# Kernel optimization log

Measured on AMD Instinct MI355X. Metric: run time of the kernel, lower is better.

## Reference

```python
import jax, jax.numpy as jnp
import numpy as np

NEG_SLOPE = 0.2


def setup_inputs() -> dict:
    key = jax.random.key(0)
    k1, k2 = jax.random.split(key)
    N, D = 8192, 64
    Wh = jax.random.normal(k1, (N, D), dtype=jnp.float32)
    # xavier_uniform on (2D, 1): bound = sqrt(6/(2D+1))
    bound = float(np.sqrt(6.0 / (2 * D + 1)))
    a = jax.random.uniform(k2, (2 * D, 1), dtype=jnp.float32, minval=-bound, maxval=bound)
    return {"Wh": Wh, "a": a}


def reference(Wh, a):
    # Original: e = LeakyReLU(cat([Wh_i, Wh_j]) @ a).view(N, N)
    # Equivalent: split a into halves; score(i,j) = Wh[i]@a1 + Wh[j]@a2.
    D = Wh.shape[1]
    a1 = a[:D, 0]  # [D]
    a2 = a[D:, 0]  # [D]
    s1 = Wh @ a1   # [N] row contribution (Wh_i)
    s2 = Wh @ a2   # [N] col contribution (Wh_j)
    e = s1[:, None] + s2[None, :]  # [N, N]
    return jnp.where(e >= 0, e, NEG_SLOPE * e)
```

## Files before the change

kernel.cpp:

```cpp
#include <hip/hip_runtime.h>

#define NEG_SLOPE 0.2f
#define D 64

__global__ __launch_bounds__(256) void gemv2_kernel(const float* __restrict__ Wh,
                                                    const float* __restrict__ a,
                                                    float* __restrict__ s,
                                                    int N) {
    const int gtid = blockIdx.x * blockDim.x + threadIdx.x;
    const int row  = gtid >> 6;
    const int lane = threadIdx.x & 63;
    if (row >= N) return;

    const float w  = Wh[row * D + lane];
    float sum1 = w * a[lane];
    float sum2 = w * a[D + lane];

    #pragma unroll
    for (int off = 32; off > 0; off >>= 1) {
        sum1 += __shfl_down(sum1, off, 64);
        sum2 += __shfl_down(sum2, off, 64);
    }
    if (lane == 0) {
        s[row]     = sum1;
        s[N + row] = sum2;
    }
}

__global__ __launch_bounds__(256) void expand_kernel(const float* __restrict__ s,
                                                     float* __restrict__ out,
                                                     int N) {
    const int row = blockIdx.y;
    const int c4  = blockIdx.x * blockDim.x + threadIdx.x;
    const float s1 = s[row];
    const float4 s2 = reinterpret_cast<const float4*>(s + N)[c4];

    float4 e;
    e.x = s1 + s2.x;
    e.y = s1 + s2.y;
    e.z = s1 + s2.z;
    e.w = s1 + s2.w;
    e.x = (e.x >= 0.f) ? e.x : NEG_SLOPE * e.x;
    e.y = (e.y >= 0.f) ? e.y : NEG_SLOPE * e.y;
    e.z = (e.z >= 0.f) ? e.z : NEG_SLOPE * e.z;
    e.w = (e.w >= 0.f) ? e.w : NEG_SLOPE * e.w;

    reinterpret_cast<float4*>(out)[(size_t)row * (N >> 2) + c4] = e;
}

extern "C" void kernel_launch(void* const* d_in, const int* in_sizes, int n_in,
                              void* d_out, int out_size, void* d_ws, size_t ws_size,
                              hipStream_t stream) {
    const float* Wh = (const float*)d_in[0];
    const float* a  = (const float*)d_in[1];
    float* out = (float*)d_out;
    float* s   = (float*)d_ws;

    const int N = in_sizes[0] / D;

    {
        const int threads = 256;
        const int blocks  = (N * 64 + threads - 1) / threads;
        gemv2_kernel<<<blocks, threads, 0, stream>>>(Wh, a, s, N);
    }

    {
        const int threads = 256;
        dim3 grid((N / 4) / threads, N);
        expand_kernel<<<grid, threads, 0, stream>>>(s, out, N);
    }
}
```

Baseline: 251.6 us.

## Fuse GEMV and outer-sum expansion into one tiled kernel with recomputed scores

Replaces the two-kernel pipeline, a GEMV that writes row and column scores to workspace and then an expansion kernel, with a single kernel over 256x256 output tiles. Each block recomputes its 256 row scores and 256 column scores from Wh in LDS, then each wave writes 64 rows of float4 outputs. This removes one launch and the workspace round trip, but every tile recomputes its dot products, so Wh is read redundantly (each row about 32 times per side). Each thread also reads Wh rows with a strided, non-coalesced pattern.

```diff
diff --git a/kernel.cpp b/kernel.cpp
--- a/kernel.cpp
+++ b/kernel.cpp
@@ -2,50 +2,61 @@
 
 #define NEG_SLOPE 0.2f
 #define D 64
+#define TILE 256
 
-__global__ __launch_bounds__(256) void gemv2_kernel(const float* __restrict__ Wh,
+__global__ __launch_bounds__(256) void fused_kernel(const float* __restrict__ Wh,
                                                     const float* __restrict__ a,
-                                                    float* __restrict__ s,
+                                                    float* __restrict__ out,
                                                     int N) {
-    const int gtid = blockIdx.x * blockDim.x + threadIdx.x;
-    const int row  = gtid >> 6;
-    const int lane = threadIdx.x & 63;
-    if (row >= N) return;
+    __shared__ float a_lds[2 * D];
+    __shared__ float s1_lds[TILE];
+    __shared__ float s2_lds[TILE];
 
-    const float w  = Wh[row * D + lane];
-    float sum1 = w * a[lane];
-    float sum2 = w * a[D + lane];
+    const int t  = threadIdx.x;
+    const int r0 = blockIdx.y * TILE;
+    const int c0 = blockIdx.x * TILE;
 
-    #pragma unroll
-    for (int off = 32; off > 0; off >>= 1) {
-        sum1 += __shfl_down(sum1, off, 64);
-        sum2 += __shfl_down(sum2, off, 64);
+    if (t < 2 * D) a_lds[t] = a[t];
+    __syncthreads();
+
+    {
+        const float4* __restrict__ wr = reinterpret_cast<const float4*>(Wh + (size_t)(r0 + t) * D);
+        const float4* __restrict__ wc = reinterpret_cast<const float4*>(Wh + (size_t)(c0 + t) * D);
+        const float4* __restrict__ a1 = reinterpret_cast<const float4*>(a_lds);
+        const float4* __restrict__ a2 = reinterpret_cast<const float4*>(a_lds + D);
+        float sum1 = 0.f, sum2 = 0.f;
+        #pragma unroll
+        for (int k = 0; k < D / 4; ++k) {
+            const float4 w1 = wr[k], v1 = a1[k];
+            sum1 += w1.x * v1.x + w1.y * v1.y + w1.z * v1.z + w1.w * v1.w;
+            const float4 w2 = wc[k], v2 = a2[k];
+            sum2 += w2.x * v2.x + w2.y * v2.y + w2.z * v2.z + w2.w * v2.w;
+        }
+        s1_lds[t] = sum1;
+        s2_lds[t] = sum2;
     }
-    if (lane == 0) {
-        s[row]     = sum1;
-        s[N + row] = sum2;
+    __syncthreads();
+
+    const int w = t >> 6;
+    const int l = t & 63;
+    const float4 s2 = reinterpret_cast<const float4*>(s2_lds)[l];
+    const int n4 = N >> 2;
+
+    #pragma unroll 4
+    for (int i = 0; i < 64; ++i) {
+        const int row = r0 + (w << 6) + i;
+        const float s1 = s1_lds[(w << 6) + i];
+        float4 e;
+        e.x = s1 + s2.x;
+        e.y = s1 + s2.y;
+        e.z = s1 + s2.z;
+        e.w = s1 + s2.w;
+        e.x = (e.x >= 0.f) ? e.x : NEG_SLOPE * e.x;
+        e.y = (e.y >= 0.f) ? e.y : NEG_SLOPE * e.y;
+        e.z = (e.z >= 0.f) ? e.z : NEG_SLOPE * e.z;
+        e.w = (e.w >= 0.f) ? e.w : NEG_SLOPE * e.w;
+        reinterpret_cast<float4*>(out)[(size_t)row * n4 + (c0 >> 2) + l] = e;
     }
-}
-
-__global__ __launch_bounds__(256) void expand_kernel(const float* __restrict__ s,
-                                                     float* __restrict__ out,
-                                                     int N) {
-    const int row = blockIdx.y;
-    const int c4  = blockIdx.x * blockDim.x + threadIdx.x;
-    const float s1 = s[row];
-    const float4 s2 = reinterpret_cast<const float4*>(s + N)[c4];
-
-    float4 e;
-    e.x = s1 + s2.x;
-    e.y = s1 + s2.y;
-    e.z = s1 + s2.z;
-    e.w = s1 + s2.w;
-    e.x = (e.x >= 0.f) ? e.x : NEG_SLOPE * e.x;
-    e.y = (e.y >= 0.f) ? e.y : NEG_SLOPE * e.y;
-    e.z = (e.z >= 0.f) ? e.z : NEG_SLOPE * e.z;
-    e.w = (e.w >= 0.f) ? e.w : NEG_SLOPE * e.w;
-
-    reinterpret_cast<float4*>(out)[(size_t)row * (N >> 2) + c4] = e;
 }
 
 extern "C" void kernel_launch(void* const* d_in, const int* in_sizes, int n_in,
@@ -54,19 +65,9 @@
     const float* Wh = (const float*)d_in[0];
     const float* a  = (const float*)d_in[1];
     float* out = (float*)d_out;
-    float* s   = (float*)d_ws;
 
     const int N = in_sizes[0] / D;
 
-    {
-        const int threads = 256;
-        const int blocks  = (N * 64 + threads - 1) / threads;
-        gemv2_kernel<<<blocks, threads, 0, stream>>>(Wh, a, s, N);
-    }
-
-    {
-        const int threads = 256;
-        dim3 grid((N / 4) / threads, N);
-        expand_kernel<<<grid, threads, 0, stream>>>(s, out, N);
-    }
+    dim3 grid(N / TILE, N / TILE);
+    fused_kernel<<<grid, TILE, 0, stream>>>(Wh, a, out, N);
 }
```

Result: slower. 262.3 us (+4.3%).
